# Optimization experiments

Hardware: AMD Instinct MI355X
Metric: run time of the kernel (lower is better)

The kernel has to match this reference:

```python
import jax, jax.numpy as jnp
import numpy as np

INPUT_DIM = 784
HIDDEN = 4096
BATCH = 64
T = 30                      # time_steps
TAU = 100.0                 # tau_mem
DECAY = 1.0 - 1.0 / TAU     # LIF leak per step
THR = 0.5                   # spike threshold
SCALE = 16.0                # input_scale
K = int(HIDDEN * 0.08)      # k-WTA k = hidden_dim * sparsity = 327


def setup_inputs() -> dict:
    key = jax.random.key(0)
    k1, k2, k3 = jax.random.split(key, 3)
    x = jax.random.uniform(k1, (BATCH, INPUT_DIM), dtype=jnp.float32)
    W1 = jax.random.normal(k2, (INPUT_DIM, HIDDEN), dtype=jnp.float32) * 0.05
    W2 = jax.random.normal(k3, (HIDDEN, HIDDEN), dtype=jnp.float32) * 0.02
    return {"x": x, "W1": W1, "W2": W2}


def _kwta(s):
    # k-WTA: keep units >= k-th largest value per row (binary spikes -> this
    # matches torch.topk kth-value thresholding; if row sum==0 it's a no-op).
    vals = jax.lax.top_k(s, K)[0]           # [B, K]
    thresh = vals[:, -1:]                   # [B, 1]
    return s * (s >= thresh).astype(s.dtype)


def _lif(v, cur):
    # Leaky integrate-and-fire: decay, integrate, hard-threshold, reset-to-zero.
    v = v * DECAY + cur
    s = (v >= THR).astype(v.dtype)
    return v * (1.0 - s), s


def reference(x, W1, W2):
    # prepare_input: normalize by max and scale (x.max()>0 branch)
    x = x / jnp.maximum(jnp.max(x), jnp.float32(1e-12)) * SCALE
    B = x.shape[0]

    def step(carry, _):
        v0, v1, v2, sum0, sum1, sum2 = carry
        v0, s0 = _lif(v0, x)                # Retina: external current each step
        v1, s1 = _lif(v1, s0 @ W1)          # V1 feedforward
        v2, s2 = _lif(v2, s1 @ W2)          # V2 feedforward
        s1m = _kwta(s1)                     # k-WTA applied to returned spikes
        s2m = _kwta(s2)
        return (v0, v1, v2, sum0 + s0, sum1 + s1m, sum2 + s2m), None

    z0 = jnp.zeros((B, INPUT_DIM), jnp.float32)
    zh = jnp.zeros((B, HIDDEN), jnp.float32)
    carry = (z0, zh, zh, z0, zh, zh)
    (_, _, _, sum0, sum1, sum2), _ = jax.lax.scan(step, carry, None, length=T)
    # mean firing rates per group (spike_sums / time_steps)
    return (sum0 / T, sum1 / T, sum2 / T)
```

## Files before the change

### kernel.cpp

```cpp
#include <hip/hip_runtime.h>
#include <cstdint>
#include <cstddef>

#define INPUT_DIM 784
#define HIDDEN    4096
#define BATCH     64
#define T_STEPS   30
#define N0 (BATCH*INPUT_DIM)
#define N1 (BATCH*HIDDEN)
#define M_ROWS (T_STEPS*BATCH)
#define NDIG 4
#define MB_CNT (M_ROWS/32)
#define KC1 25
#define KC2 128

typedef int v4i  __attribute__((ext_vector_type(4)));
typedef int v16i __attribute__((ext_vector_type(16)));

__global__ __launch_bounds__(256) void max_kernel(const float* __restrict__ x,
                                                  unsigned* __restrict__ maxbits) {
    int i = blockIdx.x * 256 + threadIdx.x;
    float v = (i < N0) ? x[i] : 0.0f;
    #pragma unroll
    for (int off = 32; off > 0; off >>= 1)
        v = fmaxf(v, __shfl_down(v, off, 64));
    __shared__ float sm[4];
    int lane = threadIdx.x & 63;
    int wv   = threadIdx.x >> 6;
    if (lane == 0) sm[wv] = v;
    __syncthreads();
    if (threadIdx.x == 0) {
        float m = fmaxf(fmaxf(sm[0], sm[1]), fmaxf(sm[2], sm[3]));
        atomicMax(maxbits, __float_as_uint(m));
    }
}

__global__ __launch_bounds__(256) void lif0_kernel(const float* __restrict__ x,
                                                   const unsigned* __restrict__ maxbits,
                                                   uint8_t* __restrict__ AF1,
                                                   float* __restrict__ out0) {
    int j = blockIdx.x * 256 + threadIdx.x;
    int b = blockIdx.y;
    if (j >= INPUT_DIM) return;
    float mx = fmaxf(__uint_as_float(*maxbits), 1e-12f);
    float xs = __fmul_rn(__fdiv_rn(x[b * INPUT_DIM + j], mx), 16.0f);
    int kc = j >> 5;
    int lane = (b & 31) | (((j >> 4) & 1) << 5);
    size_t base = (((size_t)(kc * MB_CNT + (b >> 5)) * 64 + lane) << 4) + (j & 15);
    float v = 0.0f;
    int cnt = 0;
    #pragma unroll
    for (int t = 0; t < T_STEPS; ++t) {
        v = __fadd_rn(__fmul_rn(v, 0.99f), xs);
        int s = (v >= 0.5f) ? 1 : 0;
        cnt += s;
        v = s ? 0.0f : v;
        AF1[base + (size_t)t * 2048] = (uint8_t)s;
    }
    out0[b * INPUT_DIM + j] = (float)cnt / 30.0f;
}

__global__ __launch_bounds__(256) void digitize_kernel(const float* __restrict__ W,
                                                       int8_t* __restrict__ BF,
                                                       int Krows, int KC, double scale) {
    __shared__ float tile[32][33];
    const int nb = blockIdx.x, kc = blockIdx.y;
    const int tid = threadIdx.x;
    {
        int r  = tid >> 3;
        int c4 = (tid & 7) << 2;
        int k  = kc * 32 + r;
        float4 w4 = make_float4(0.f, 0.f, 0.f, 0.f);
        if (k < Krows)
            w4 = *(const float4*)&W[(size_t)k * HIDDEN + nb * 32 + c4];
        tile[r][c4]     = w4.x;
        tile[r][c4 + 1] = w4.y;
        tile[r][c4 + 2] = w4.z;
        tile[r][c4 + 3] = w4.w;
    }
    __syncthreads();
    const int d    = tid >> 6;
    const int lane = tid & 63;
    const int nl   = lane & 31;
    const int kh   = (lane >> 5) << 4;
    char dig[16];
    #pragma unroll
    for (int jj = 0; jj < 16; ++jj) {
        double w = (double)tile[kh + jj][nl];
        long long q = __double2ll_rn(w * scale);
        int dd = 0;
        #pragma unroll
        for (int dd_i = 0; dd_i <= 3; ++dd_i) {
            dd = (int)(((q + 128) & 255) - 128);
            q = (q - (long long)dd) >> 8;
            if (dd_i == d) break;
        }
        dig[jj] = (char)dd;
    }
    *(int4*)&BF[((((size_t)nb * KC + kc) * NDIG + d) << 10) + (lane << 4)] =
        *(int4*)&dig[0];
}

#define MFMA_GRP(A0, A1, B0, B1, B2, B3)                                        \
    acc[0][0] = __builtin_amdgcn_mfma_i32_32x32x32_i8(A0, B0, acc[0][0], 0, 0, 0); \
    acc[1][0] = __builtin_amdgcn_mfma_i32_32x32x32_i8(A1, B0, acc[1][0], 0, 0, 0); \
    acc[0][1] = __builtin_amdgcn_mfma_i32_32x32x32_i8(A0, B1, acc[0][1], 0, 0, 0); \
    acc[1][1] = __builtin_amdgcn_mfma_i32_32x32x32_i8(A1, B1, acc[1][1], 0, 0, 0); \
    acc[0][2] = __builtin_amdgcn_mfma_i32_32x32x32_i8(A0, B2, acc[0][2], 0, 0, 0); \
    acc[1][2] = __builtin_amdgcn_mfma_i32_32x32x32_i8(A1, B2, acc[1][2], 0, 0, 0); \
    acc[0][3] = __builtin_amdgcn_mfma_i32_32x32x32_i8(A0, B3, acc[0][3], 0, 0, 0); \
    acc[1][3] = __builtin_amdgcn_mfma_i32_32x32x32_i8(A1, B3, acc[1][3], 0, 0, 0)

#define LOAD_SLOT(S)                                                            \
    As[S][0] = *(const v4i*)ap;          As[S][1] = *(const v4i*)(ap + 1024);   \
    Bs[S][0] = *(const v4i*)bp;          Bs[S][1] = *(const v4i*)(bp + 1024);   \
    Bs[S][2] = *(const v4i*)(bp + 2048); Bs[S][3] = *(const v4i*)(bp + 3072)

#define MFMA_SLOT(S) MFMA_GRP(As[S][0], As[S][1], Bs[S][0], Bs[S][1], Bs[S][2], Bs[S][3])

template <int KC>
__global__ __launch_bounds__(256, 2) void gemm_i8_kernel(const int8_t* __restrict__ AF,
                                                         const int8_t* __restrict__ BF,
                                                         double* __restrict__ C,
                                                         double scale) {
    const int tid  = threadIdx.x;
    const int wave = tid >> 6, lane = tid & 63;
    const int i  = blockIdx.x;
    const int p  = (i >= 480) ? 1 : 0;
    const int j  = i - p * 480;
    const int bx = j >> 5;
    const int by = p * 32 + ((j & 7) << 2) + ((j >> 3) & 3);
    const int nb  = by * 2 + (wave & 1);
    const int msb = (wave >> 1) * 2;
    const int mb0 = bx * 4 + msb;

    const int8_t* ap = AF + (((size_t)mb0 * 64 + lane) << 4);
    const int8_t* bp = BF + (((size_t)nb * KC * NDIG) << 10) + (lane << 4);
    const int astride = MB_CNT * 64 * 16;
    const int bstride = NDIG * 1024;

    v16i acc[2][4] = {};
    v4i As[2][2], Bs[2][4];

    LOAD_SLOT(0);
    ap += astride; bp += bstride;
    LOAD_SLOT(1);

    constexpr int KCE = (KC - 2) & ~1;
    #pragma unroll 2
    for (int kc = 0; kc < KCE; ++kc) {
        const int s = kc & 1;
        if (s == 0) { MFMA_SLOT(0); } else { MFMA_SLOT(1); }
        ap += astride; bp += bstride;
        if (s == 0) { LOAD_SLOT(0); } else { LOAD_SLOT(1); }
    }

    if constexpr ((KC & 1) == 0) {
        MFMA_SLOT(0);
        MFMA_SLOT(1);
    } else {
        MFMA_SLOT(0);
        ap += astride; bp += bstride;
        LOAD_SLOT(0);
        MFMA_SLOT(1);
        MFMA_SLOT(0);
    }

    const int col = lane & 31;
    const int rb  = (lane >> 5) << 2;
    const int n_g = by * 64 + (wave & 1) * 32 + col;
    #pragma unroll
    for (int s = 0; s < 2; ++s) {
        const int m_base = bx * 128 + (msb + s) * 32;
        #pragma unroll
        for (int r = 0; r < 16; ++r) {
            int row = (r & 3) + 8 * (r >> 2) + rb;
            long long v = 0;
            #pragma unroll
            for (int d = 3; d >= 0; --d) v = (v << 8) + (long long)acc[s][d][r];
            C[(size_t)(m_base + row) * HIDDEN + n_g] = (double)v * scale;
        }
    }
}

__global__ __launch_bounds__(256) void lif1_kernel(const double* __restrict__ CUR,
                                                   uint8_t* __restrict__ AF,
                                                   float* __restrict__ out1) {
    int e = blockIdx.x * 256 + threadIdx.x;
    int b = e >> 12;
    int j = e & 4095;
    int kc = j >> 5;
    int lane = (b & 31) | (((j >> 4) & 1) << 5);
    size_t base = (((size_t)(kc * MB_CNT + (b >> 5)) * 64 + lane) << 4) + (j & 15);
    double v = 0.0;
    int cnt = 0;
    #pragma unroll
    for (int t = 0; t < T_STEPS; ++t) {
        double cur = CUR[(size_t)t * N1 + e];
        v = __dadd_rn(__dmul_rn(v, 0.99), cur);
        int s = (v >= 0.5) ? 1 : 0;
        cnt += s;
        v = s ? 0.0 : v;
        AF[base + (size_t)t * 2048] = (uint8_t)s;
    }
    out1[e] = (float)cnt / 30.0f;
}

__global__ __launch_bounds__(256) void lif2_kernel(const double* __restrict__ CUR,
                                                   float* __restrict__ out2) {
    int e = blockIdx.x * 256 + threadIdx.x;
    double v = 0.0;
    int cnt = 0;
    #pragma unroll
    for (int t = 0; t < T_STEPS; ++t) {
        double cur = CUR[(size_t)t * N1 + e];
        v = __dadd_rn(__dmul_rn(v, 0.99), cur);
        int s = (v >= 0.5) ? 1 : 0;
        cnt += s;
        v = s ? 0.0 : v;
    }
    out2[e] = (float)cnt / 30.0f;
}

extern "C" void kernel_launch(void* const* d_in, const int* in_sizes, int n_in,
                              void* d_out, int out_size, void* d_ws, size_t ws_size,
                              hipStream_t stream) {
    const float* x  = (const float*)d_in[0];
    const float* W1 = (const float*)d_in[1];
    const float* W2 = (const float*)d_in[2];
    float* out = (float*)d_out;
    char*  ws  = (char*)d_ws;

    const size_t AF1_SZ = (size_t)KC1 * MB_CNT * 1024;
    const size_t BF1_SZ = (size_t)128 * KC1 * NDIG * 1024;
    const size_t AF2_SZ = (size_t)KC2 * MB_CNT * 1024;
    const size_t BF2_SZ = (size_t)128 * KC2 * NDIG * 1024;
    unsigned* maxbits = (unsigned*)ws;
    uint8_t*  AF1 = (uint8_t*)(ws + 256);
    int8_t*   BF1 = (int8_t*)(AF1 + AF1_SZ);
    uint8_t*  AF2 = (uint8_t*)(BF1 + BF1_SZ);
    int8_t*   BF2 = (int8_t*)(AF2 + AF2_SZ);
    double*   CURd = (double*)((char*)BF2 + BF2_SZ);

    float* out0 = out;
    float* out1 = out + N0;
    float* out2 = out + N0 + N1;

    hipMemsetAsync(maxbits, 0, 4, stream);
    hipMemsetAsync(AF1, 0, AF1_SZ, stream);
    max_kernel <<<(N0 + 255) / 256, 256, 0, stream>>>(x, maxbits);
    lif0_kernel<<<dim3(4, BATCH), 256, 0, stream>>>(x, maxbits, AF1, out0);
    digitize_kernel<<<dim3(128, KC1), 256, 0, stream>>>(W1, BF1, INPUT_DIM, KC1,
                                                        4294967296.0);
    digitize_kernel<<<dim3(128, KC2), 256, 0, stream>>>(W2, BF2, HIDDEN, KC2,
                                                        8589934592.0);
    gemm_i8_kernel<KC1><<<960, 256, 0, stream>>>((const int8_t*)AF1, BF1, CURd,
                                                 2.3283064365386963e-10);
    lif1_kernel<<<N1 / 256, 256, 0, stream>>>(CURd, AF2, out1);
    gemm_i8_kernel<KC2><<<960, 256, 0, stream>>>((const int8_t*)AF2, BF2, CURd,
                                                 1.1641532182693481e-10);
    lif2_kernel<<<N1 / 256, 256, 0, stream>>>(CURd, out2);
}
```

Baseline: 327.5 us.

## Stage GEMM operand tiles through LDS with async global_load_lds double buffering

Replaces the per-wave direct global register loads of A and B fragments with cooperative block-wide global_load_lds copies into a double-buffered shared-memory tile. Each tile is now fetched from global once per block and shared, where before the waves sharing an A or B fragment each loaded it separately. The cost is extra barriers and waitcnt synchronisation per k-chunk, plus LDS reads, which may limit overlap between loads and MFMA.

```diff
diff --git a/kernel.cpp b/kernel.cpp
--- a/kernel.cpp
+++ b/kernel.cpp
@@ -111,18 +111,41 @@
     acc[0][3] = __builtin_amdgcn_mfma_i32_32x32x32_i8(A0, B3, acc[0][3], 0, 0, 0); \
     acc[1][3] = __builtin_amdgcn_mfma_i32_32x32x32_i8(A1, B3, acc[1][3], 0, 0, 0)
 
-#define LOAD_SLOT(S)                                                            \
-    As[S][0] = *(const v4i*)ap;          As[S][1] = *(const v4i*)(ap + 1024);   \
-    Bs[S][0] = *(const v4i*)bp;          Bs[S][1] = *(const v4i*)(bp + 1024);   \
-    Bs[S][2] = *(const v4i*)(bp + 2048); Bs[S][3] = *(const v4i*)(bp + 3072)
-
-#define MFMA_SLOT(S) MFMA_GRP(As[S][0], As[S][1], Bs[S][0], Bs[S][1], Bs[S][2], Bs[S][3])
+__device__ __forceinline__ void gload16(const int8_t* g, int8_t* l) {
+    __builtin_amdgcn_global_load_lds(
+        (const __attribute__((address_space(1))) void*)g,
+        (__attribute__((address_space(3))) void*)l, 16, 0, 0);
+}
+
+#define STAGE(BUF, KCV)                                                          \
+    do {                                                                         \
+        gload16(gA  + (size_t)(KCV) * astride, &lds[BUF][       (wave << 10)]);  \
+        gload16(gB0 + (size_t)(KCV) * bstride, &lds[BUF][4096 + (wave << 10)]);  \
+        gload16(gB1 + (size_t)(KCV) * bstride, &lds[BUF][8192 + (wave << 10)]);  \
+    } while (0)
+
+#define ITER(S, WN, DOSTAGE, KCV)                                                \
+    do {                                                                         \
+        asm volatile("s_waitcnt vmcnt(" #WN ")" ::: "memory");                   \
+        __builtin_amdgcn_s_barrier();                                            \
+        v4i a0 = *(const v4i*)&lds[S][ msb      * 1024 + (lane << 4)];           \
+        v4i a1 = *(const v4i*)&lds[S][(msb + 1) * 1024 + (lane << 4)];           \
+        v4i b0 = *(const v4i*)&lds[S][4096 + ((wave & 1) << 12) +        (lane << 4)]; \
+        v4i b1 = *(const v4i*)&lds[S][4096 + ((wave & 1) << 12) + 1024 + (lane << 4)]; \
+        v4i b2 = *(const v4i*)&lds[S][4096 + ((wave & 1) << 12) + 2048 + (lane << 4)]; \
+        v4i b3 = *(const v4i*)&lds[S][4096 + ((wave & 1) << 12) + 3072 + (lane << 4)]; \
+        asm volatile("s_waitcnt lgkmcnt(0)" ::: "memory");                       \
+        __builtin_amdgcn_s_barrier();                                            \
+        if (DOSTAGE) { STAGE(S, (KCV) + 2); }                                    \
+        MFMA_GRP(a0, a1, b0, b1, b2, b3);                                        \
+    } while (0)
 
 template <int KC>
 __global__ __launch_bounds__(256, 2) void gemm_i8_kernel(const int8_t* __restrict__ AF,
                                                          const int8_t* __restrict__ BF,
                                                          double* __restrict__ C,
                                                          double scale) {
+    __shared__ int8_t lds[2][12288];
     const int tid  = threadIdx.x;
     const int wave = tid >> 6, lane = tid & 63;
     const int i  = blockIdx.x;
@@ -130,40 +153,32 @@
     const int j  = i - p * 480;
     const int bx = j >> 5;
     const int by = p * 32 + ((j & 7) << 2) + ((j >> 3) & 3);
-    const int nb  = by * 2 + (wave & 1);
+    const int nb0 = by * 2;
     const int msb = (wave >> 1) * 2;
-    const int mb0 = bx * 4 + msb;
-
-    const int8_t* ap = AF + (((size_t)mb0 * 64 + lane) << 4);
-    const int8_t* bp = BF + (((size_t)nb * KC * NDIG) << 10) + (lane << 4);
-    const int astride = MB_CNT * 64 * 16;
+
+    const int astride = MB_CNT * 1024;
     const int bstride = NDIG * 1024;
+    const int8_t* gA  = AF + (((size_t)(bx * 4) * 64) << 4) + tid * 16;
+    const int8_t* gB0 = BF + (((size_t)nb0 * KC * NDIG) << 10) + tid * 16;
+    const int8_t* gB1 = gB0 + ((size_t)KC * NDIG << 10);
 
     v16i acc[2][4] = {};
-    v4i As[2][2], Bs[2][4];
-
-    LOAD_SLOT(0);
-    ap += astride; bp += bstride;
-    LOAD_SLOT(1);
-
-    constexpr int KCE = (KC - 2) & ~1;
-    #pragma unroll 2
-    for (int kc = 0; kc < KCE; ++kc) {
-        const int s = kc & 1;
-        if (s == 0) { MFMA_SLOT(0); } else { MFMA_SLOT(1); }
-        ap += astride; bp += bstride;
-        if (s == 0) { LOAD_SLOT(0); } else { LOAD_SLOT(1); }
-    }
-
+
+    STAGE(0, 0);
+    STAGE(1, 1);
+
+    constexpr int KCM = (KC - 2) & ~1;
+    for (int kc = 0; kc < KCM; kc += 2) {
+        ITER(0, 3, 1, kc);
+        ITER(1, 3, 1, kc + 1);
+    }
     if constexpr ((KC & 1) == 0) {
-        MFMA_SLOT(0);
-        MFMA_SLOT(1);
+        ITER(0, 3, 0, KC - 2);
+        ITER(1, 0, 0, KC - 1);
     } else {
-        MFMA_SLOT(0);
-        ap += astride; bp += bstride;
-        LOAD_SLOT(0);
-        MFMA_SLOT(1);
-        MFMA_SLOT(0);
+        ITER(0, 3, 1, KC - 3);
+        ITER(1, 3, 0, KC - 2);
+        ITER(0, 0, 0, KC - 1);
     }
 
     const int col = lane & 31;
```

After: 305.6 us. 1.07x faster.
